# Kernel optimization log

Measured on AMD Instinct MI355X. Metric: run time of the kernel, lower is better.

Reference implementation:

```python
import jax, jax.numpy as jnp
import numpy as np

STATE_MASS = 4.0
EPS = 1e-5
LOW_RANK_SCALE = 0.1  # _LOW_RANK_SCALE_INIT


def _ln(x, g, b):
    mu = jnp.mean(x, axis=-1, keepdims=True)
    var = jnp.var(x, axis=-1, keepdims=True)
    return (x - mu) * jax.lax.rsqrt(var + EPS) * g + b


def _signed_abs_softmax(s, axis=-1):
    s = jnp.nan_to_num(s)
    return jnp.sign(s) * jax.nn.softmax(jnp.abs(s), axis=axis)


def _signed_softmax_state(st):
    st = jnp.nan_to_num(st)
    return jnp.sign(st) * jax.nn.softmax(jnp.abs(st), axis=-1) * STATE_MASS


def _low_rank_scores(dst, src, Ut_w, Ut_b, Us_w, Us_b, w):
    # bilinear low-rank pairwise: score[b,i,j] = sum_r (dst_i Ut)_r * w_r * (src_j Us)_r
    pt = dst @ Ut_w + Ut_b                      # [B,Nd,R]
    ps = src @ Us_w + Us_b                      # [B,Ns,R]
    return jnp.einsum('bir,r,bjr->bij', pt, w * LOW_RANK_SCALE, ps)


def _gather_rows(x, idx):
    # x: [B,N,...], idx: [B,M,K] -> [B,M,K,...] (per-batch gather, no NxM broadcast)
    return jax.vmap(lambda xi, ii: xi[ii])(x, idx)


def setup_inputs() -> dict:
    key = jax.random.key(0)
    ks = jax.random.split(key, 8)
    B, S, D, M, R = 16, 2048, 512, 256, 64
    std = 0.02
    return {
        'token_val': jax.random.normal(ks[0], (B, S, D), jnp.float32),
        'token_state': jax.random.normal(ks[1], (B, S), jnp.float32),
        'init_state': jax.random.normal(ks[2], (M,), jnp.float32) * std,
        'init_val': jax.random.normal(ks[3], (M, D), jnp.float32) * std,
        'rUs_w': jax.random.normal(ks[4], (D, R), jnp.float32) * std,
        'rUs_b': jnp.zeros((R,), jnp.float32),
        'rUt_w': jax.random.normal(ks[5], (D, R), jnp.float32) * std,
        'rUt_b': jnp.zeros((R,), jnp.float32),
        'r_w': jnp.ones((R,), jnp.float32),
        'pUs_w': jax.random.normal(ks[6], (D, R), jnp.float32) * std,
        'pUs_b': jnp.zeros((R,), jnp.float32),
        'pUt_w': jax.random.normal(ks[7], (D, R), jnp.float32) * std,
        'pUt_b': jnp.zeros((R,), jnp.float32),
        'p_w': jnp.ones((R,), jnp.float32),
        'ln_g': jnp.ones((D,), jnp.float32),
        'ln_b': jnp.zeros((D,), jnp.float32),
        'topk': 16,
    }


def reference(token_val, token_state, init_state, init_val,
              rUs_w, rUs_b, rUt_w, rUt_b, r_w,
              pUs_w, pUs_b, pUt_w, pUt_b, p_w,
              ln_g, ln_b, topk):
    B = token_val.shape[0]
    M, D = init_val.shape

    # _MemoryLevel.initialize
    mem_state = _signed_softmax_state(jnp.broadcast_to(init_state, (B, M)))
    mem_val = _ln(jnp.broadcast_to(init_val, (B, M, D)), ln_g, ln_b)

    # ---- SparseTransition (write): route tokens -> slots, top-k sources/slot ----
    scores = _low_rank_scores(mem_val, token_val, rUt_w, rUt_b, rUs_w, rUs_b, r_w)  # [B,M,S]
    _, idx = jax.lax.top_k(jnp.abs(scores), topk)              # [B,M,K]
    sel = jnp.take_along_axis(scores, idx, axis=-1)            # [B,M,K]
    edges = _signed_abs_softmax(sel, axis=-1)                  # signed-abs-softmax over edges
    v_sel = _gather_rows(token_val, idx)                       # [B,M,K,D]
    s_sel = _gather_rows(token_state, idx)                     # [B,M,K]
    mem_val = mem_val + jnp.einsum('bmk,bmkd->bmd', edges, v_sel)   # merge_mode='add'
    mem_state = mem_state + jnp.einsum('bmk,bmk->bm', edges, s_sel)
    mem_state = _signed_softmax_state(mem_state)
    mem_val = _ln(mem_val, ln_g, ln_b)

    # ---- SparsePropagation within slots: state-weighted top-k edges, residual ----
    pscores = _low_rank_scores(mem_val, mem_val, pUt_w, pUt_b, pUs_w, pUs_b, p_w)   # [B,M,M]
    pscores = pscores * mem_state[:, None, :]                  # state_weight_edges
    _, pidx = jax.lax.top_k(jnp.abs(pscores), topk)            # [B,M,K]
    psel = jnp.take_along_axis(pscores, pidx, axis=-1)
    pe = _signed_abs_softmax(psel, axis=-1)
    pv = _gather_rows(mem_val, pidx)                           # [B,M,K,D]
    pst = _gather_rows(mem_state, pidx)                        # [B,M,K]
    mem_val = mem_val + jnp.einsum('bmk,bmkd->bmd', pe, pv)    # residual=True
    mem_state = mem_state + jnp.einsum('bmk,bmk->bm', pe, pst)
    mem_state = _signed_softmax_state(mem_state)
    mem_val = _ln(mem_val, ln_g, ln_b)
    return mem_val
```

## Files before the change

kernel.cpp:

```cpp
#include <hip/hip_runtime.h>
#include <hip/hip_bf16.h>
#include <math.h>

#define BB 16
#define SS 2048
#define DD 512
#define MM 256
#define RR 64
#define KK 16
#define GPAD 68

__device__ __forceinline__ float wave_sum(float v) {
#pragma unroll
  for (int off = 32; off > 0; off >>= 1) v += __shfl_xor(v, off);
  return v;
}

__device__ __forceinline__ float sgnf(float v) {
  return (v > 0.f) ? 1.f : ((v < 0.f) ? -1.f : 0.f);
}

__global__ __launch_bounds__(256) void k_init(
    const float* __restrict__ init_val, const float* __restrict__ ln_g,
    const float* __restrict__ ln_b, const float* __restrict__ rUt_w,
    const float* __restrict__ rUt_b, const float* __restrict__ r_w,
    float* __restrict__ mv0, float* __restrict__ pt0) {
  int m = blockIdx.x, t = threadIdx.x;
  __shared__ float row[DD];
  __shared__ float red[8];
  float x0 = init_val[m * DD + t];
  float x1 = init_val[m * DD + t + 256];
  float s = wave_sum(x0 + x1);
  float sq = wave_sum(x0 * x0 + x1 * x1);
  if ((t & 63) == 0) { red[t >> 6] = s; red[4 + (t >> 6)] = sq; }
  __syncthreads();
  float mean = (red[0] + red[1] + red[2] + red[3]) * (1.0f / DD);
  float var = (red[4] + red[5] + red[6] + red[7]) * (1.0f / DD) - mean * mean;
  float rs = rsqrtf(var + 1e-5f);
  float n0 = (x0 - mean) * rs * ln_g[t] + ln_b[t];
  float n1 = (x1 - mean) * rs * ln_g[t + 256] + ln_b[t + 256];
  mv0[m * DD + t] = n0;
  mv0[m * DD + t + 256] = n1;
  row[t] = n0;
  row[t + 256] = n1;
  __syncthreads();
  if (t < RR) {
    float acc = rUt_b[t];
    for (int d = 0; d < DD; ++d) acc += row[d] * rUt_w[d * RR + t];
    pt0[m * RR + t] = acc * r_w[t] * 0.1f;
  }
}

__global__ __launch_bounds__(256) void k_state_softmax(
    const float* __restrict__ in, float* __restrict__ out) {
  int b = blockIdx.x, t = threadIdx.x;
  __shared__ float red[4];
  float v = in[b * MM + t];
  float a = fabsf(v);
  float mx = a;
#pragma unroll
  for (int off = 32; off > 0; off >>= 1) mx = fmaxf(mx, __shfl_xor(mx, off));
  if ((t & 63) == 0) red[t >> 6] = mx;
  __syncthreads();
  mx = fmaxf(fmaxf(red[0], red[1]), fmaxf(red[2], red[3]));
  __syncthreads();
  float e = expf(a - mx);
  float ssum = wave_sum(e);
  if ((t & 63) == 0) red[t >> 6] = ssum;
  __syncthreads();
  ssum = red[0] + red[1] + red[2] + red[3];
  out[b * MM + t] = sgnf(v) * e / ssum * 4.0f;
}

template <bool TRANS_OUT>
__device__ __forceinline__ void gemm_body(
    const float* __restrict__ A, const float* __restrict__ W,
    const float* __restrict__ bias, const float* __restrict__ colscale,
    float csmul, const float* __restrict__ rowscale, float* __restrict__ C,
    int row0, float (*Ast)[GPAD], float (*Ws)[GPAD]) {
  int tid = threadIdx.x;
  int ty = tid >> 4, tx = tid & 15;
  float acc[4][4] = {};
  for (int kc = 0; kc < DD; kc += 32) {
#pragma unroll
    for (int i = 0; i < 2; ++i) {
      int s4 = i * 256 + tid;
      int r = s4 >> 3;
      int k4 = s4 & 7;
      float4 v = *reinterpret_cast<const float4*>(
          &A[(size_t)(row0 + r) * DD + kc + k4 * 4]);
      Ast[k4 * 4 + 0][r] = v.x;
      Ast[k4 * 4 + 1][r] = v.y;
      Ast[k4 * 4 + 2][r] = v.z;
      Ast[k4 * 4 + 3][r] = v.w;
    }
#pragma unroll
    for (int i = 0; i < 2; ++i) {
      int s4 = i * 256 + tid;
      int r = s4 >> 4;
      int c4 = s4 & 15;
      float4 v = *reinterpret_cast<const float4*>(
          &W[(size_t)(kc + r) * RR + c4 * 4]);
      *reinterpret_cast<float4*>(&Ws[r][c4 * 4]) = v;
    }
    __syncthreads();
#pragma unroll
    for (int k = 0; k < 32; ++k) {
      float4 a4 = *reinterpret_cast<const float4*>(&Ast[k][ty * 4]);
      float4 w4 = *reinterpret_cast<const float4*>(&Ws[k][tx * 4]);
      acc[0][0] += a4.x * w4.x; acc[0][1] += a4.x * w4.y;
      acc[0][2] += a4.x * w4.z; acc[0][3] += a4.x * w4.w;
      acc[1][0] += a4.y * w4.x; acc[1][1] += a4.y * w4.y;
      acc[1][2] += a4.y * w4.z; acc[1][3] += a4.y * w4.w;
      acc[2][0] += a4.z * w4.x; acc[2][1] += a4.z * w4.y;
      acc[2][2] += a4.z * w4.z; acc[2][3] += a4.z * w4.w;
      acc[3][0] += a4.w * w4.x; acc[3][1] += a4.w * w4.y;
      acc[3][2] += a4.w * w4.z; acc[3][3] += a4.w * w4.w;
    }
    __syncthreads();
  }
#pragma unroll
  for (int i = 0; i < 4; ++i) {
    int rr = row0 + ty * 4 + i;
    float rsc = rowscale ? rowscale[rr] : 1.f;
    if (TRANS_OUT) {
#pragma unroll
      for (int j = 0; j < 4; ++j) {
        int cc = tx * 4 + j;
        float v = acc[i][j] + bias[cc];
        if (colscale) v *= colscale[cc] * csmul;
        v *= rsc;
        C[((size_t)(rr >> 8) * RR + cc) * MM + (rr & 255)] = v;
      }
    } else {
      float4 o;
      float b0 = bias[tx * 4], b1 = bias[tx * 4 + 1];
      float b2 = bias[tx * 4 + 2], b3 = bias[tx * 4 + 3];
      o.x = acc[i][0] + b0; o.y = acc[i][1] + b1;
      o.z = acc[i][2] + b2; o.w = acc[i][3] + b3;
      if (colscale) {
        o.x *= colscale[tx * 4] * csmul; o.y *= colscale[tx * 4 + 1] * csmul;
        o.z *= colscale[tx * 4 + 2] * csmul; o.w *= colscale[tx * 4 + 3] * csmul;
      }
      o.x *= rsc; o.y *= rsc; o.z *= rsc; o.w *= rsc;
      *reinterpret_cast<float4*>(&C[(size_t)rr * RR + tx * 4]) = o;
    }
  }
}

__global__ __launch_bounds__(256) void k_gemm_skinny(
    const float* __restrict__ A, const float* __restrict__ W,
    const float* __restrict__ bias, float* __restrict__ C) {
  __shared__ float Ast[32][GPAD];
  __shared__ float Ws[32][GPAD];
  gemm_body<false>(A, W, bias, nullptr, 1.f, nullptr, C, blockIdx.x * 64,
                   Ast, Ws);
}

__global__ __launch_bounds__(256) void k_gemm_pair(
    const float* __restrict__ mv1, const float* __restrict__ pUt_w,
    const float* __restrict__ pUt_b, const float* __restrict__ p_w,
    const float* __restrict__ pUs_w, const float* __restrict__ pUs_b,
    const float* __restrict__ ms1, float* __restrict__ pt1,
    float* __restrict__ ps1T) {
  __shared__ float Ast[32][GPAD];
  __shared__ float Ws[32][GPAD];
  if (blockIdx.x < 64) {
    gemm_body<false>(mv1, pUt_w, pUt_b, p_w, 0.1f, nullptr, pt1,
                     blockIdx.x * 64, Ast, Ws);
  } else {
    gemm_body<true>(mv1, pUs_w, pUs_b, nullptr, 1.f, ms1, ps1T,
                    (blockIdx.x - 64) * 64, Ast, Ws);
  }
}

__global__ __launch_bounds__(256) void k_scores(
    const float* __restrict__ pt0, const float* __restrict__ ps,
    float* __restrict__ scores) {
  int b = blockIdx.z;
  int m0 = blockIdx.y * 64;
  int j0 = blockIdx.x * 64;
  __shared__ float Pt[64][65];
  __shared__ float Ps[64][65];
  int tid = threadIdx.x;
  int ty = tid >> 4, tx = tid & 15;
#pragma unroll
  for (int i = 0; i < 4; ++i) {
    int idx4 = i * 256 + tid;
    int r = idx4 >> 4;
    int c = (idx4 & 15) << 2;
    float4 vp = *reinterpret_cast<const float4*>(&pt0[(size_t)(m0 + r) * RR + c]);
    Pt[r][c] = vp.x; Pt[r][c + 1] = vp.y; Pt[r][c + 2] = vp.z; Pt[r][c + 3] = vp.w;
    float4 vs = *reinterpret_cast<const float4*>(
        &ps[((size_t)b * SS + j0 + r) * RR + c]);
    Ps[r][c] = vs.x; Ps[r][c + 1] = vs.y; Ps[r][c + 2] = vs.z; Ps[r][c + 3] = vs.w;
  }
  __syncthreads();
  float acc[4][4] = {};
#pragma unroll
  for (int k = 0; k < 64; ++k) {
    float a0 = Pt[ty * 4 + 0][k], a1 = Pt[ty * 4 + 1][k];
    float a2 = Pt[ty * 4 + 2][k], a3 = Pt[ty * 4 + 3][k];
    float b0 = Ps[tx * 4 + 0][k], b1 = Ps[tx * 4 + 1][k];
    float b2 = Ps[tx * 4 + 2][k], b3 = Ps[tx * 4 + 3][k];
    acc[0][0] += a0 * b0; acc[0][1] += a0 * b1; acc[0][2] += a0 * b2; acc[0][3] += a0 * b3;
    acc[1][0] += a1 * b0; acc[1][1] += a1 * b1; acc[1][2] += a1 * b2; acc[1][3] += a1 * b3;
    acc[2][0] += a2 * b0; acc[2][1] += a2 * b1; acc[2][2] += a2 * b2; acc[2][3] += a2 * b3;
    acc[3][0] += a3 * b0; acc[3][1] += a3 * b1; acc[3][2] += a3 * b2; acc[3][3] += a3 * b3;
  }
  float* obase = scores + (size_t)b * MM * SS;
#pragma unroll
  for (int i = 0; i < 4; ++i) {
#pragma unroll
    for (int j = 0; j < 4; ++j) {
      obase[(size_t)(m0 + ty * 4 + i) * SS + j0 + tx * 4 + j] = acc[i][j];
    }
  }
}

__global__ __launch_bounds__(256) void k_write(
    const float* __restrict__ scores, const float* __restrict__ token_val,
    const float* __restrict__ token_state, const float* __restrict__ mv0,
    const float* __restrict__ ms0, const float* __restrict__ ln_g,
    const float* __restrict__ ln_b, float* __restrict__ mv1,
    float* __restrict__ ms_w) {
  int t = threadIdx.x;
  int wave = t >> 6, lane = t & 63;
  int i = blockIdx.x;
  int slot = i >> 3;
  int b = 2 * (i & 7) + (slot >> 6);
  int m = (slot & 63) * 4 + wave;
  int row = b * MM + m;
  __shared__ float srl[4][SS];
  __shared__ int selj_sh[4][KK];
  float4* srl4 = reinterpret_cast<float4*>(&srl[wave][0]);
  const float* srow = scores + (size_t)row * SS;
  unsigned maxa = 0u;
#pragma unroll
  for (int ch = 0; ch < 8; ++ch) {
    float4 q = *reinterpret_cast<const float4*>(srow + (ch * 64 + lane) * 4);
    srl4[ch * 64 + lane] = q;
    maxa = max(maxa, __float_as_uint(q.x) & 0x7fffffffu);
    maxa = max(maxa, __float_as_uint(q.y) & 0x7fffffffu);
    maxa = max(maxa, __float_as_uint(q.z) & 0x7fffffffu);
    maxa = max(maxa, __float_as_uint(q.w) & 0x7fffffffu);
  }
#pragma unroll
  for (int off = 32; off > 0; off >>= 1)
    maxa = max(maxa, (unsigned)__shfl_xor((int)maxa, off));
  unsigned lo = 0u, hi = maxa, thr = 0u;
  bool early = false;
  while (lo < hi) {
    unsigned mid = lo + ((hi - lo + 1u) >> 1);
    int cnt = 0;
#pragma unroll
    for (int ch = 0; ch < 8; ++ch) {
      float4 q = srl4[ch * 64 + lane];
      cnt += __popcll(__ballot((__float_as_uint(q.x) & 0x7fffffffu) >= mid));
      cnt += __popcll(__ballot((__float_as_uint(q.y) & 0x7fffffffu) >= mid));
      cnt += __popcll(__ballot((__float_as_uint(q.z) & 0x7fffffffu) >= mid));
      cnt += __popcll(__ballot((__float_as_uint(q.w) & 0x7fffffffu) >= mid));
    }
    if (cnt == KK) { thr = mid; early = true; break; }
    if (cnt > KK) lo = mid; else hi = mid - 1u;
  }
  if (!early) thr = lo;
  unsigned long long ltmask = (1ull << lane) - 1ull;
  int s = 0;
  unsigned tiemask = 0u;
#pragma unroll
  for (int ch = 0; ch < 8; ++ch) {
    float4 q = srl4[ch * 64 + lane];
    unsigned a4[4] = {__float_as_uint(q.x) & 0x7fffffffu,
                      __float_as_uint(q.y) & 0x7fffffffu,
                      __float_as_uint(q.z) & 0x7fffffffu,
                      __float_as_uint(q.w) & 0x7fffffffu};
#pragma unroll
    for (int cc = 0; cc < 4; ++cc) {
      bool sg = early ? (a4[cc] >= thr) : (a4[cc] > thr);
      unsigned long long mk = __ballot(sg);
      if (sg) selj_sh[wave][s + __popcll(mk & ltmask)] = ch * 256 + lane * 4 + cc;
      s += __popcll(mk);
      if (!early && a4[cc] == thr) tiemask |= 1u << (ch * 4 + cc);
    }
  }
  int taken = s;
  while (taken < KK) {
    int myj = 0x7fffffff;
#pragma unroll
    for (int c = 0; c < 32; ++c)
      if ((tiemask >> c) & 1u) {
        int j = (c >> 2) * 256 + lane * 4 + (c & 3);
        myj = min(myj, j);
      }
    int wj = myj;
#pragma unroll
    for (int off = 32; off > 0; off >>= 1) wj = min(wj, __shfl_xor(wj, off));
    if (wj == 0x7fffffff) break;
    if (((wj >> 2) & 63) == lane) tiemask &= ~(1u << (((wj >> 8) << 2) | (wj & 3)));
    if (lane == 0) selj_sh[wave][taken] = wj;
    ++taken;
  }
  int js[KK];
  float es[KK];
#pragma unroll
  for (int k = 0; k < KK; ++k) {
    js[k] = selj_sh[wave][k];
    es[k] = srl[wave][js[k]];
  }
  float mx = 0.f;
#pragma unroll
  for (int k = 0; k < KK; ++k) mx = fmaxf(mx, fabsf(es[k]));
  float ssum = 0.f;
#pragma unroll
  for (int k = 0; k < KK; ++k) {
    float ex = expf(fabsf(es[k]) - mx);
    ssum += ex;
    es[k] = sgnf(es[k]) * ex;
  }
  float inv = 1.f / ssum;
  int dbase = lane * 8;
  const float* m0row = mv0 + m * DD + dbase;
  float4 a0 = *reinterpret_cast<const float4*>(m0row);
  float4 a1 = *reinterpret_cast<const float4*>(m0row + 4);
  float acc[8] = {a0.x, a0.y, a0.z, a0.w, a1.x, a1.y, a1.z, a1.w};
  float stacc = 0.f;
#pragma unroll
  for (int k = 0; k < KK; ++k) {
    float e = es[k] * inv;
    const float* tv = token_val + ((size_t)b * SS + js[k]) * DD + dbase;
    float4 u0 = *reinterpret_cast<const float4*>(tv);
    float4 u1 = *reinterpret_cast<const float4*>(tv + 4);
    acc[0] += e * u0.x; acc[1] += e * u0.y; acc[2] += e * u0.z; acc[3] += e * u0.w;
    acc[4] += e * u1.x; acc[5] += e * u1.y; acc[6] += e * u1.z; acc[7] += e * u1.w;
    stacc += e * token_state[(size_t)b * SS + js[k]];
  }
  if (lane == 0) ms_w[row] = ms0[m] + stacc;
  float s1 = 0.f, s2 = 0.f;
#pragma unroll
  for (int c = 0; c < 8; ++c) { s1 += acc[c]; s2 += acc[c] * acc[c]; }
  s1 = wave_sum(s1);
  s2 = wave_sum(s2);
  float mean = s1 * (1.0f / DD);
  float var = s2 * (1.0f / DD) - mean * mean;
  float rs = rsqrtf(var + 1e-5f);
  float4 g0 = *reinterpret_cast<const float4*>(ln_g + dbase);
  float4 g1 = *reinterpret_cast<const float4*>(ln_g + dbase + 4);
  float4 b0v = *reinterpret_cast<const float4*>(ln_b + dbase);
  float4 b1v = *reinterpret_cast<const float4*>(ln_b + dbase + 4);
  float4 o0, o1;
  o0.x = (acc[0] - mean) * rs * g0.x + b0v.x;
  o0.y = (acc[1] - mean) * rs * g0.y + b0v.y;
  o0.z = (acc[2] - mean) * rs * g0.z + b0v.z;
  o0.w = (acc[3] - mean) * rs * g0.w + b0v.w;
  o1.x = (acc[4] - mean) * rs * g1.x + b1v.x;
  o1.y = (acc[5] - mean) * rs * g1.y + b1v.y;
  o1.z = (acc[6] - mean) * rs * g1.z + b1v.z;
  o1.w = (acc[7] - mean) * rs * g1.w + b1v.w;
  float* orow = mv1 + (size_t)row * DD + dbase;
  *reinterpret_cast<float4*>(orow) = o0;
  *reinterpret_cast<float4*>(orow + 4) = o1;
}

__global__ __launch_bounds__(256, 4) void k_prop(
    const float* __restrict__ pt1, const float* __restrict__ ps1T,
    const float* __restrict__ mv1, const float* __restrict__ ln_g,
    const float* __restrict__ ln_b, float* __restrict__ out) {
  int t = threadIdx.x;
  int wave = t >> 6, lane = t & 63;
  int row = blockIdx.x * 4 + wave;
  int b = row >> 8, m = row & 255;
  __shared__ int selj_sh[4][KK];
  __shared__ float selv_sh[4][KK];
  float ptval = pt1[(size_t)row * RR + lane];
  const float* pB = ps1T + (size_t)b * RR * MM + lane * 4;
  float sc[4] = {0.f, 0.f, 0.f, 0.f};
#pragma unroll 8
  for (int r = 0; r < RR; ++r) {
    float w = __shfl(ptval, r);
    float4 pv = *reinterpret_cast<const float4*>(pB + r * MM);
    sc[0] += w * pv.x; sc[1] += w * pv.y; sc[2] += w * pv.z; sc[3] += w * pv.w;
  }
  int jbase = lane * 4;
  unsigned au[4];
#pragma unroll
  for (int c = 0; c < 4; ++c) au[c] = __float_as_uint(sc[c]) & 0x7fffffffu;
  unsigned lo = 0u, hi = 0x7f800000u, thr = 0u;
  bool early = false;
  while (lo < hi) {
    unsigned mid = lo + ((hi - lo + 1u) >> 1);
    int cnt = 0;
#pragma unroll
    for (int c = 0; c < 4; ++c) cnt += __popcll(__ballot(au[c] >= mid));
    if (cnt == KK) { thr = mid; early = true; break; }
    if (cnt > KK) lo = mid; else hi = mid - 1u;
  }
  if (!early) thr = lo;
  unsigned long long ltmask = (1ull << lane) - 1ull;
  int s = 0;
  unsigned tiemask = 0u;
#pragma unroll
  for (int c = 0; c < 4; ++c) {
    bool sg = early ? (au[c] >= thr) : (au[c] > thr);
    unsigned long long mk = __ballot(sg);
    if (sg) {
      int slot = s + __popcll(mk & ltmask);
      selj_sh[wave][slot] = jbase + c;
      selv_sh[wave][slot] = sc[c];
    }
    s += __popcll(mk);
    if (!early && au[c] == thr) tiemask |= 1u << c;
  }
  int taken = s;
  while (taken < KK) {
    int myj = 0x7fffffff;
#pragma unroll
    for (int c = 0; c < 4; ++c)
      if ((tiemask >> c) & 1u) myj = min(myj, jbase + c);
    int wj = myj;
#pragma unroll
    for (int off = 32; off > 0; off >>= 1) wj = min(wj, __shfl_xor(wj, off));
    if (wj == 0x7fffffff) break;
    if (wj >= jbase && wj < jbase + 4) {
      tiemask &= ~(1u << (wj - jbase));
      selv_sh[wave][taken] = sc[wj - jbase];
      if (lane == (wj >> 2)) selj_sh[wave][taken] = wj;
    }
    ++taken;
  }
  int js[KK];
  float es[KK];
#pragma unroll
  for (int k = 0; k < KK; ++k) { js[k] = selj_sh[wave][k]; es[k] = selv_sh[wave][k]; }
  float mx = 0.f;
#pragma unroll
  for (int k = 0; k < KK; ++k) mx = fmaxf(mx, fabsf(es[k]));
  float ssum = 0.f;
#pragma unroll
  for (int k = 0; k < KK; ++k) {
    float ex = expf(fabsf(es[k]) - mx);
    ssum += ex;
    es[k] = sgnf(es[k]) * ex;
  }
  float inv = 1.f / ssum;
  int dbase = lane * 8;
  const float* mrow = mv1 + (size_t)row * DD + dbase;
  float4 a0 = *reinterpret_cast<const float4*>(mrow);
  float4 a1 = *reinterpret_cast<const float4*>(mrow + 4);
  float acc[8] = {a0.x, a0.y, a0.z, a0.w, a1.x, a1.y, a1.z, a1.w};
#pragma unroll
  for (int k = 0; k < KK; ++k) {
    float e = es[k] * inv;
    const float* pv = mv1 + ((size_t)b * MM + js[k]) * DD + dbase;
    float4 u0 = *reinterpret_cast<const float4*>(pv);
    float4 u1 = *reinterpret_cast<const float4*>(pv + 4);
    acc[0] += e * u0.x; acc[1] += e * u0.y; acc[2] += e * u0.z; acc[3] += e * u0.w;
    acc[4] += e * u1.x; acc[5] += e * u1.y; acc[6] += e * u1.z; acc[7] += e * u1.w;
  }
  float s1 = 0.f, s2 = 0.f;
#pragma unroll
  for (int c = 0; c < 8; ++c) { s1 += acc[c]; s2 += acc[c] * acc[c]; }
  s1 = wave_sum(s1);
  s2 = wave_sum(s2);
  float mean = s1 * (1.0f / DD);
  float var = s2 * (1.0f / DD) - mean * mean;
  float rs = rsqrtf(var + 1e-5f);
  float4 g0 = *reinterpret_cast<const float4*>(ln_g + dbase);
  float4 g1 = *reinterpret_cast<const float4*>(ln_g + dbase + 4);
  float4 b0v = *reinterpret_cast<const float4*>(ln_b + dbase);
  float4 b1v = *reinterpret_cast<const float4*>(ln_b + dbase + 4);
  float4 o0, o1;
  o0.x = (acc[0] - mean) * rs * g0.x + b0v.x;
  o0.y = (acc[1] - mean) * rs * g0.y + b0v.y;
  o0.z = (acc[2] - mean) * rs * g0.z + b0v.z;
  o0.w = (acc[3] - mean) * rs * g0.w + b0v.w;
  o1.x = (acc[4] - mean) * rs * g1.x + b1v.x;
  o1.y = (acc[5] - mean) * rs * g1.y + b1v.y;
  o1.z = (acc[6] - mean) * rs * g1.z + b1v.z;
  o1.w = (acc[7] - mean) * rs * g1.w + b1v.w;
  float* orow = out + (size_t)row * DD + dbase;
  *reinterpret_cast<float4*>(orow) = o0;
  *reinterpret_cast<float4*>(orow + 4) = o1;
}

extern "C" void kernel_launch(void* const* d_in, const int* in_sizes, int n_in,
                              void* d_out, int out_size, void* d_ws,
                              size_t ws_size, hipStream_t stream) {
  const float* token_val = (const float*)d_in[0];
  const float* token_state = (const float*)d_in[1];
  const float* init_state = (const float*)d_in[2];
  const float* init_val = (const float*)d_in[3];
  const float* rUs_w = (const float*)d_in[4];
  const float* rUs_b = (const float*)d_in[5];
  const float* rUt_w = (const float*)d_in[6];
  const float* rUt_b = (const float*)d_in[7];
  const float* r_w = (const float*)d_in[8];
  const float* pUs_w = (const float*)d_in[9];
  const float* pUs_b = (const float*)d_in[10];
  const float* pUt_w = (const float*)d_in[11];
  const float* pUt_b = (const float*)d_in[12];
  const float* p_w = (const float*)d_in[13];
  const float* ln_g = (const float*)d_in[14];
  const float* ln_b = (const float*)d_in[15];
  float* out = (float*)d_out;

  float* ws = (float*)d_ws;
  float* mv0 = ws;    ws += MM * DD;
  float* pt0 = ws;    ws += MM * RR;
  float* ms0 = ws;    ws += MM;
  float* ps = ws;     ws += (size_t)BB * SS * RR;
  float* scores = ws; ws += (size_t)BB * MM * SS;
  float* mv1 = ws;    ws += (size_t)BB * MM * DD;
  float* ms_w = ws;   ws += BB * MM;
  float* ms1 = ws;    ws += BB * MM;
  float* pt1 = ws;    ws += (size_t)BB * MM * RR;
  float* ps1T = ws;   ws += (size_t)BB * RR * MM;

  k_init<<<MM, 256, 0, stream>>>(init_val, ln_g, ln_b, rUt_w, rUt_b, r_w, mv0, pt0);
  k_state_softmax<<<1, 256, 0, stream>>>(init_state, ms0);
  k_gemm_skinny<<<(BB * SS) / 64, 256, 0, stream>>>(token_val, rUs_w, rUs_b, ps);
  dim3 gs(SS / 64, MM / 64, BB);
  k_scores<<<gs, 256, 0, stream>>>(pt0, ps, scores);
  k_write<<<(BB * MM) / 4, 256, 0, stream>>>(scores, token_val, token_state,
                                             mv0, ms0, ln_g, ln_b, mv1, ms_w);
  k_state_softmax<<<BB, 256, 0, stream>>>(ms_w, ms1);
  k_gemm_pair<<<128, 256, 0, stream>>>(mv1, pUt_w, pUt_b, p_w, pUs_w, pUs_b,
                                       ms1, pt1, ps1T);
  k_prop<<<(BB * MM) / 4, 256, 0, stream>>>(pt1, ps1T, mv1, ln_g, ln_b, out);
}
```

Baseline: 162.5 us.

## Retile token projection and scores GEMMs with register prefetch and transposed smem

Replaces the skinny token projection GEMM with a dedicated kernel using 128-row tiles, 8x4 per-thread outputs and register prefetch of the next K chunk, so global loads overlap the FMA loop. The scores kernel now uses 64x128 tiles with K-major transposed shared memory, padded to avoid bank conflicts, and float4 reads and stores instead of strided scalar accesses. The shared gemm_body epilogue is simplified to scalar stores. This trades more registers per thread and fewer blocks for better reuse and vectorized memory traffic.

```diff
diff --git a/kernel.cpp b/kernel.cpp
--- a/kernel.cpp
+++ b/kernel.cpp
@@ -72,6 +72,91 @@
   out[b * MM + t] = sgnf(v) * e / ssum * 4.0f;
 }
 
+__global__ __launch_bounds__(256) void k_ps(
+    const float* __restrict__ A, const float* __restrict__ W,
+    const float* __restrict__ bias, float* __restrict__ C) {
+  __shared__ float Ast[32][128];
+  __shared__ float Ws[32][RR];
+  int t = threadIdx.x;
+  int tx = t & 15;
+  int ty = t >> 4;
+  int row0 = blockIdx.x * 128;
+  float4 ra[4];
+  float4 rw[2];
+#pragma unroll
+  for (int i = 0; i < 4; ++i) {
+    int slot = i * 256 + t;
+    int r = slot >> 3, k4 = slot & 7;
+    ra[i] = *reinterpret_cast<const float4*>(&A[(size_t)(row0 + r) * DD + k4 * 4]);
+  }
+#pragma unroll
+  for (int i = 0; i < 2; ++i) {
+    int slot = i * 256 + t;
+    int k = slot >> 4, c4 = slot & 15;
+    rw[i] = *reinterpret_cast<const float4*>(&W[(size_t)k * RR + c4 * 4]);
+  }
+  float acc[8][4] = {};
+  for (int c = 0; c < 16; ++c) {
+    __syncthreads();
+#pragma unroll
+    for (int i = 0; i < 4; ++i) {
+      int slot = i * 256 + t;
+      int r = slot >> 3, k4 = slot & 7;
+      Ast[k4 * 4 + 0][r] = ra[i].x;
+      Ast[k4 * 4 + 1][r] = ra[i].y;
+      Ast[k4 * 4 + 2][r] = ra[i].z;
+      Ast[k4 * 4 + 3][r] = ra[i].w;
+    }
+#pragma unroll
+    for (int i = 0; i < 2; ++i) {
+      int slot = i * 256 + t;
+      int k = slot >> 4, c4 = slot & 15;
+      *reinterpret_cast<float4*>(&Ws[k][c4 * 4]) = rw[i];
+    }
+    __syncthreads();
+    if (c < 15) {
+      int kc = (c + 1) * 32;
+#pragma unroll
+      for (int i = 0; i < 4; ++i) {
+        int slot = i * 256 + t;
+        int r = slot >> 3, k4 = slot & 7;
+        ra[i] = *reinterpret_cast<const float4*>(
+            &A[(size_t)(row0 + r) * DD + kc + k4 * 4]);
+      }
+#pragma unroll
+      for (int i = 0; i < 2; ++i) {
+        int slot = i * 256 + t;
+        int k = slot >> 4, c4 = slot & 15;
+        rw[i] = *reinterpret_cast<const float4*>(
+            &W[(size_t)(kc + k) * RR + c4 * 4]);
+      }
+    }
+#pragma unroll
+    for (int k = 0; k < 32; ++k) {
+      float4 alo = *reinterpret_cast<const float4*>(&Ast[k][ty * 8]);
+      float4 ahi = *reinterpret_cast<const float4*>(&Ast[k][ty * 8 + 4]);
+      float4 w4 = *reinterpret_cast<const float4*>(&Ws[k][tx * 4]);
+      acc[0][0] += alo.x * w4.x; acc[0][1] += alo.x * w4.y; acc[0][2] += alo.x * w4.z; acc[0][3] += alo.x * w4.w;
+      acc[1][0] += alo.y * w4.x; acc[1][1] += alo.y * w4.y; acc[1][2] += alo.y * w4.z; acc[1][3] += alo.y * w4.w;
+      acc[2][0] += alo.z * w4.x; acc[2][1] += alo.z * w4.y; acc[2][2] += alo.z * w4.z; acc[2][3] += alo.z * w4.w;
+      acc[3][0] += alo.w * w4.x; acc[3][1] += alo.w * w4.y; acc[3][2] += alo.w * w4.z; acc[3][3] += alo.w * w4.w;
+      acc[4][0] += ahi.x * w4.x; acc[4][1] += ahi.x * w4.y; acc[4][2] += ahi.x * w4.z; acc[4][3] += ahi.x * w4.w;
+      acc[5][0] += ahi.y * w4.x; acc[5][1] += ahi.y * w4.y; acc[5][2] += ahi.y * w4.z; acc[5][3] += ahi.y * w4.w;
+      acc[6][0] += ahi.z * w4.x; acc[6][1] += ahi.z * w4.y; acc[6][2] += ahi.z * w4.z; acc[6][3] += ahi.z * w4.w;
+      acc[7][0] += ahi.w * w4.x; acc[7][1] += ahi.w * w4.y; acc[7][2] += ahi.w * w4.z; acc[7][3] += ahi.w * w4.w;
+    }
+  }
+  float4 bv = *reinterpret_cast<const float4*>(&bias[tx * 4]);
+#pragma unroll
+  for (int r = 0; r < 8; ++r) {
+    int rr = row0 + ty * 8 + r;
+    float4 o;
+    o.x = acc[r][0] + bv.x; o.y = acc[r][1] + bv.y;
+    o.z = acc[r][2] + bv.z; o.w = acc[r][3] + bv.w;
+    *reinterpret_cast<float4*>(&C[(size_t)rr * RR + tx * 4]) = o;
+  }
+}
+
 template <bool TRANS_OUT>
 __device__ __forceinline__ void gemm_body(
     const float* __restrict__ A, const float* __restrict__ W,
@@ -123,38 +208,19 @@
   for (int i = 0; i < 4; ++i) {
     int rr = row0 + ty * 4 + i;
     float rsc = rowscale ? rowscale[rr] : 1.f;
-    if (TRANS_OUT) {
-#pragma unroll
-      for (int j = 0; j < 4; ++j) {
-        int cc = tx * 4 + j;
-        float v = acc[i][j] + bias[cc];
-        if (colscale) v *= colscale[cc] * csmul;
-        v *= rsc;
+#pragma unroll
+    for (int j = 0; j < 4; ++j) {
+      int cc = tx * 4 + j;
+      float v = acc[i][j] + bias[cc];
+      if (colscale) v *= colscale[cc] * csmul;
+      v *= rsc;
+      if (TRANS_OUT) {
         C[((size_t)(rr >> 8) * RR + cc) * MM + (rr & 255)] = v;
+      } else {
+        C[(size_t)rr * RR + cc] = v;
       }
-    } else {
-      float4 o;
-      float b0 = bias[tx * 4], b1 = bias[tx * 4 + 1];
-      float b2 = bias[tx * 4 + 2], b3 = bias[tx * 4 + 3];
-      o.x = acc[i][0] + b0; o.y = acc[i][1] + b1;
-      o.z = acc[i][2] + b2; o.w = acc[i][3] + b3;
-      if (colscale) {
-        o.x *= colscale[tx * 4] * csmul; o.y *= colscale[tx * 4 + 1] * csmul;
-        o.z *= colscale[tx * 4 + 2] * csmul; o.w *= colscale[tx * 4 + 3] * csmul;
-      }
-      o.x *= rsc; o.y *= rsc; o.z *= rsc; o.w *= rsc;
-      *reinterpret_cast<float4*>(&C[(size_t)rr * RR + tx * 4]) = o;
-    }
-  }
-}
-
-__global__ __launch_bounds__(256) void k_gemm_skinny(
-    const float* __restrict__ A, const float* __restrict__ W,
-    const float* __restrict__ bias, float* __restrict__ C) {
-  __shared__ float Ast[32][GPAD];
-  __shared__ float Ws[32][GPAD];
-  gemm_body<false>(A, W, bias, nullptr, 1.f, nullptr, C, blockIdx.x * 64,
-                   Ast, Ws);
+    }
+  }
 }
 
 __global__ __launch_bounds__(256) void k_gemm_pair(
@@ -174,47 +240,83 @@
   }
 }
 
+#define PSW 144
+__device__ __forceinline__ int psw(int j) { return j + ((j >> 5) << 2); }
+
 __global__ __launch_bounds__(256) void k_scores(
     const float* __restrict__ pt0, const float* __restrict__ ps,
     float* __restrict__ scores) {
+  __shared__ float PtT[RR][64];
+  __shared__ float PsT[RR][PSW];
+  int t = threadIdx.x;
   int b = blockIdx.z;
   int m0 = blockIdx.y * 64;
-  int j0 = blockIdx.x * 64;
-  __shared__ float Pt[64][65];
-  __shared__ float Ps[64][65];
-  int tid = threadIdx.x;
-  int ty = tid >> 4, tx = tid & 15;
+  int j0 = blockIdx.x * 128;
+  {
+    int tm4 = t >> 4, tk4 = t & 15;
+    const float* base = pt0 + (size_t)(m0 + tm4 * 4) * RR + tk4 * 4;
+    float4 v0 = *reinterpret_cast<const float4*>(base);
+    float4 v1 = *reinterpret_cast<const float4*>(base + RR);
+    float4 v2 = *reinterpret_cast<const float4*>(base + 2 * RR);
+    float4 v3 = *reinterpret_cast<const float4*>(base + 3 * RR);
+    float4 w;
+    w.x = v0.x; w.y = v1.x; w.z = v2.x; w.w = v3.x;
+    *reinterpret_cast<float4*>(&PtT[tk4 * 4 + 0][tm4 * 4]) = w;
+    w.x = v0.y; w.y = v1.y; w.z = v2.y; w.w = v3.y;
+    *reinterpret_cast<float4*>(&PtT[tk4 * 4 + 1][tm4 * 4]) = w;
+    w.x = v0.z; w.y = v1.z; w.z = v2.z; w.w = v3.z;
+    *reinterpret_cast<float4*>(&PtT[tk4 * 4 + 2][tm4 * 4]) = w;
+    w.x = v0.w; w.y = v1.w; w.z = v2.w; w.w = v3.w;
+    *reinterpret_cast<float4*>(&PtT[tk4 * 4 + 3][tm4 * 4]) = w;
+  }
+#pragma unroll
+  for (int ii = 0; ii < 2; ++ii) {
+    int slot = ii * 256 + t;
+    int jt = slot >> 4, kt = slot & 15;
+    const float* base = ps + ((size_t)b * SS + j0 + jt * 4) * RR + kt * 4;
+    float4 v0 = *reinterpret_cast<const float4*>(base);
+    float4 v1 = *reinterpret_cast<const float4*>(base + RR);
+    float4 v2 = *reinterpret_cast<const float4*>(base + 2 * RR);
+    float4 v3 = *reinterpret_cast<const float4*>(base + 3 * RR);
+    int jc = psw(jt * 4);
+    float4 w;
+    w.x = v0.x; w.y = v1.x; w.z = v2.x; w.w = v3.x;
+    *reinterpret_cast<float4*>(&PsT[kt * 4 + 0][jc]) = w;
+    w.x = v0.y; w.y = v1.y; w.z = v2.y; w.w = v3.y;
+    *reinterpret_cast<float4*>(&PsT[kt * 4 + 1][jc]) = w;
+    w.x = v0.z; w.y = v1.z; w.z = v2.z; w.w = v3.z;
+    *reinterpret_cast<float4*>(&PsT[kt * 4 + 2][jc]) = w;
+    w.x = v0.w; w.y = v1.w; w.z = v2.w; w.w = v3.w;
+    *reinterpret_cast<float4*>(&PsT[kt * 4 + 3][jc]) = w;
+  }
+  __syncthreads();
+  int tj = t & 15;
+  int tm = t >> 4;
+  int jlo = psw(tj * 8);
+  int jhi = psw(tj * 8 + 4);
+  float acc[4][8] = {};
+#pragma unroll
+  for (int k = 0; k < RR; ++k) {
+    float4 a4 = *reinterpret_cast<const float4*>(&PtT[k][tm * 4]);
+    float4 w0 = *reinterpret_cast<const float4*>(&PsT[k][jlo]);
+    float4 w1 = *reinterpret_cast<const float4*>(&PsT[k][jhi]);
+    acc[0][0] += a4.x * w0.x; acc[0][1] += a4.x * w0.y; acc[0][2] += a4.x * w0.z; acc[0][3] += a4.x * w0.w;
+    acc[0][4] += a4.x * w1.x; acc[0][5] += a4.x * w1.y; acc[0][6] += a4.x * w1.z; acc[0][7] += a4.x * w1.w;
+    acc[1][0] += a4.y * w0.x; acc[1][1] += a4.y * w0.y; acc[1][2] += a4.y * w0.z; acc[1][3] += a4.y * w0.w;
+    acc[1][4] += a4.y * w1.x; acc[1][5] += a4.y * w1.y; acc[1][6] += a4.y * w1.z; acc[1][7] += a4.y * w1.w;
+    acc[2][0] += a4.z * w0.x; acc[2][1] += a4.z * w0.y; acc[2][2] += a4.z * w0.z; acc[2][3] += a4.z * w0.w;
+    acc[2][4] += a4.z * w1.x; acc[2][5] += a4.z * w1.y; acc[2][6] += a4.z * w1.z; acc[2][7] += a4.z * w1.w;
+    acc[3][0] += a4.w * w0.x; acc[3][1] += a4.w * w0.y; acc[3][2] += a4.w * w0.z; acc[3][3] += a4.w * w0.w;
+    acc[3][4] += a4.w * w1.x; acc[3][5] += a4.w * w1.y; acc[3][6] += a4.w * w1.z; acc[3][7] += a4.w * w1.w;
+  }
+  float* obase = scores + (size_t)b * MM * SS + (size_t)(m0 + tm * 4) * SS + j0 + tj * 8;
 #pragma unroll
   for (int i = 0; i < 4; ++i) {
-    int idx4 = i * 256 + tid;
-    int r = idx4 >> 4;
-    int c = (idx4 & 15) << 2;
-    float4 vp = *reinterpret_cast<const float4*>(&pt0[(size_t)(m0 + r) * RR + c]);
-    Pt[r][c] = vp.x; Pt[r][c + 1] = vp.y; Pt[r][c + 2] = vp.z; Pt[r][c + 3] = vp.w;
-    float4 vs = *reinterpret_cast<const float4*>(
-        &ps[((size_t)b * SS + j0 + r) * RR + c]);
-    Ps[r][c] = vs.x; Ps[r][c + 1] = vs.y; Ps[r][c + 2] = vs.z; Ps[r][c + 3] = vs.w;
-  }
-  __syncthreads();
-  float acc[4][4] = {};
-#pragma unroll
-  for (int k = 0; k < 64; ++k) {
-    float a0 = Pt[ty * 4 + 0][k], a1 = Pt[ty * 4 + 1][k];
-    float a2 = Pt[ty * 4 + 2][k], a3 = Pt[ty * 4 + 3][k];
-    float b0 = Ps[tx * 4 + 0][k], b1 = Ps[tx * 4 + 1][k];
-    float b2 = Ps[tx * 4 + 2][k], b3 = Ps[tx * 4 + 3][k];
-    acc[0][0] += a0 * b0; acc[0][1] += a0 * b1; acc[0][2] += a0 * b2; acc[0][3] += a0 * b3;
-    acc[1][0] += a1 * b0; acc[1][1] += a1 * b1; acc[1][2] += a1 * b2; acc[1][3] += a1 * b3;
-    acc[2][0] += a2 * b0; acc[2][1] += a2 * b1; acc[2][2] += a2 * b2; acc[2][3] += a2 * b3;
-    acc[3][0] += a3 * b0; acc[3][1] += a3 * b1; acc[3][2] += a3 * b2; acc[3][3] += a3 * b3;
-  }
-  float* obase = scores + (size_t)b * MM * SS;
-#pragma unroll
-  for (int i = 0; i < 4; ++i) {
-#pragma unroll
-    for (int j = 0; j < 4; ++j) {
-      obase[(size_t)(m0 + ty * 4 + i) * SS + j0 + tx * 4 + j] = acc[i][j];
-    }
+    float4 o0, o1;
+    o0.x = acc[i][0]; o0.y = acc[i][1]; o0.z = acc[i][2]; o0.w = acc[i][3];
+    o1.x = acc[i][4]; o1.y = acc[i][5]; o1.z = acc[i][6]; o1.w = acc[i][7];
+    *reinterpret_cast<float4*>(obase + (size_t)i * SS) = o0;
+    *reinterpret_cast<float4*>(obase + (size_t)i * SS + 4) = o1;
   }
 }
 
@@ -518,8 +620,8 @@
 
   k_init<<<MM, 256, 0, stream>>>(init_val, ln_g, ln_b, rUt_w, rUt_b, r_w, mv0, pt0);
   k_state_softmax<<<1, 256, 0, stream>>>(init_state, ms0);
-  k_gemm_skinny<<<(BB * SS) / 64, 256, 0, stream>>>(token_val, rUs_w, rUs_b, ps);
-  dim3 gs(SS / 64, MM / 64, BB);
+  k_ps<<<(BB * SS) / 128, 256, 0, stream>>>(token_val, rUs_w, rUs_b, ps);
+  dim3 gs(SS / 128, MM / 64, BB);
   k_scores<<<gs, 256, 0, stream>>>(pt0, ps, scores);
   k_write<<<(BB * MM) / 4, 256, 0, stream>>>(scores, token_val, token_state,
                                              mv0, ms0, ln_g, ln_b, mv1, ms_w);
```

Result: slower. 173.8 us (+7.0%).
